# Optimization experiments

Measured on AMD Instinct MI355X. Metric: run time of the kernel, lower is better.

## Reference

```python
import jax, jax.numpy as jnp
import numpy as np

# Config matching init_kwargs: input_shape=(512,512,28), stride=2
M, N, L = 512, 512, 28
STRIDE = 2
B = 8


def setup_inputs() -> dict:
    key = jax.random.key(0)
    kx, kp = jax.random.split(key)
    x = jax.random.normal(kx, (B, L, M, N), dtype=jnp.float32)
    # phi = (1 + sign(randn)) / 2  -> binary {0,1} mask of shape (M, N)
    phi = (jax.random.normal(kp, (M, N)) > 0).astype(jnp.float32)
    return {"x": x, "phi": phi}


def reference(x, phi):
    """CASSI forward: get_transpose(get_measurement(x, phi), phi, mask_mul=True).

    x:   (b, L, M, N) hyperspectral cube
    phi: (M, N) coded aperture, broadcast across L bands
    """
    b, l, m, n = x.shape
    n_out = n + STRIDE * (l - 1)

    # --- get_measurement: mask-multiply then per-band shift-and-accumulate ---
    y1 = x * phi[None, None, :, :]                      # (b, L, M, N)
    # column index each (band, col) lands in after dispersion shift
    scat_idx = (STRIDE * jnp.arange(l)[:, None] + jnp.arange(n)[None, :]).reshape(-1)  # (L*N,)
    y1f = y1.transpose(0, 2, 1, 3).reshape(b, m, l * n)  # (b, M, L*N)
    y2 = jnp.zeros((b, m, n_out), dtype=x.dtype).at[:, :, scat_idx].add(y1f)  # (b, M, Nout)
    # y_norm=False: no normalization

    # --- get_transpose: gather shifted windows (width = y.shape[-2] = M) ---
    gat_idx = STRIDE * jnp.arange(l)[:, None] + jnp.arange(m)[None, :]  # (L, M)
    xt = y2[:, :, gat_idx]             # (b, M, L, M)
    xt = jnp.moveaxis(xt, 2, 1)        # (b, L, M, M)
    return xt * phi[None, None, :, :]  # mask_mul=True
```

## Files before the change

### kernel.cpp

```cpp
#include <hip/hip_runtime.h>


#define M_DIM 512
#define N_DIM 512
#define L_DIM 28
#define B_DIM 8
#define MN_DIM (M_DIM * N_DIM)
#define NT 14
#define U_DIM 14

typedef float v2f __attribute__((ext_vector_type(2)));
typedef float v4f __attribute__((ext_vector_type(4)));

__global__ __launch_bounds__(128) void cassi_fwd_kernel(
    const float* __restrict__ x, const float* __restrict__ phi,
    float* __restrict__ out)
{
    __shared__ __align__(16) float sphi[N_DIM];
    __shared__ __align__(16) float sy2[576];

    const int t  = threadIdx.x;
    const int bm = blockIdx.x;
    const int b  = bm >> 9;
    const int m  = bm & 511;

    const float* xrow = x + (size_t)b * L_DIM * MN_DIM + (size_t)m * N_DIM;

    v4f pq = *(const v4f*)(phi + (size_t)m * N_DIM + 4 * t);
    *(v4f*)&sphi[4 * t] = pq;
    __syncthreads();

    const bool lane0 = ((t & 63) == 0);

    v4f acc  = {0.f, 0.f, 0.f, 0.f};
    v4f acct = {0.f, 0.f, 0.f, 0.f};

#pragma unroll
    for (int u = 0; u < U_DIM; ++u) {
        const int s  = t - u;
        const int sc = s < 0 ? 0 : s;
        const float* re = xrow + (size_t)(2 * u) * MN_DIM;
        const float* ro = xrow + (size_t)(2 * u + 1) * MN_DIM;
        v4f xe = *(const v4f*)(re + 4 * sc);
        v4f xo = *(const v4f*)(ro + 4 * sc);
        v4f P  = *(const v4f*)(&sphi[4 * sc]);
        v4f ze = xe * P;
        v4f zo = xo * P;

        if (s >= 0) acc += ze;

        float lo0 = __shfl_up(zo.z, 1, 64);
        float lo1 = __shfl_up(zo.w, 1, 64);
        if (lane0 && s >= 1) {
            v2f xl = *(const v2f*)(ro + 4 * s - 2);
            v2f pl = *(const v2f*)(&sphi[4 * s - 2]);
            lo0 = xl.x * pl.x;
            lo1 = xl.y * pl.y;
        }
        if (s >= 1) { acc.x += lo0;  acc.y += lo1; }
        if (s >= 0) { acc.z += zo.x; acc.w += zo.y; }

        if (t < NT) {
            if (u == t) {
                v2f xl = *(const v2f*)(ro + 510);
                v2f pl = *(const v2f*)(&sphi[510]);
                acct.x += xl.x * pl.x;
                acct.y += xl.y * pl.y;
            } else if (u > t) {
                const int n0 = 512 + 4 * t - 4 * u;
                v4f xte = *(const v4f*)(re + n0);
                v4f Pt  = *(const v4f*)(&sphi[n0]);
                acct += xte * Pt;
                v2f xa = *(const v2f*)(ro + n0 - 2);
                v2f pa = *(const v2f*)(&sphi[n0 - 2]);
                v2f xb = *(const v2f*)(ro + n0);
                acct.x += xa.x * pa.x;
                acct.y += xa.y * pa.y;
                acct.z += xb.x * Pt.x;
                acct.w += xb.y * Pt.y;
            }
        }
    }

    *(v4f*)&sy2[4 * t] = acc;
    if (t < NT) *(v4f*)&sy2[512 + 4 * t] = acct;
    __syncthreads();

    float* orow = out + (size_t)b * L_DIM * MN_DIM + (size_t)m * N_DIM;
    const float* sy = &sy2[0];
#pragma unroll
    for (int l = 0; l < L_DIM; ++l) {
        v2f ya = *(const v2f*)(sy + 2 * l + 4 * t);
        v2f yb = *(const v2f*)(sy + 2 * l + 4 * t + 2);
        v4f o;
        o.x = pq.x * ya.x;
        o.y = pq.y * ya.y;
        o.z = pq.z * yb.x;
        o.w = pq.w * yb.y;
        __builtin_nontemporal_store(o, (v4f*)(orow + (size_t)l * MN_DIM + 4 * t));
    }
}

extern "C" void kernel_launch(void* const* d_in, const int* in_sizes, int n_in,
                              void* d_out, int out_size, void* d_ws, size_t ws_size,
                              hipStream_t stream) {
    const float* x   = (const float*)d_in[0];
    const float* phi = (const float*)d_in[1];
    float* out       = (float*)d_out;
    cassi_fwd_kernel<<<dim3(B_DIM * M_DIM), dim3(128), 0, stream>>>(x, phi, out);
}
```

Baseline: 393.8 us.

## Split fused kernel into y2 reduction pass and separate expand pass via workspace

Splits the fused kernel into two. The first kernel computes the dispersed measurement rows y2 and writes them to a workspace buffer. The second kernel reads y2 and phi and writes each output band, with blocks ordered by band so that consecutive stores are contiguous. The goal is more streaming-friendly write patterns and more parallelism in the expand phase, at the cost of an extra kernel launch and a round trip of y2 through global memory. If the workspace is missing or too small, the original fused kernel runs instead.

```diff
diff --git a/kernel.cpp b/kernel.cpp
--- a/kernel.cpp
+++ b/kernel.cpp
@@ -8,16 +8,17 @@
 #define MN_DIM (M_DIM * N_DIM)
 #define NT 14
 #define U_DIM 14
+#define YSTRIDE 576
+#define MB 8
 
 typedef float v2f __attribute__((ext_vector_type(2)));
 typedef float v4f __attribute__((ext_vector_type(4)));
 
-__global__ __launch_bounds__(128) void cassi_fwd_kernel(
+__global__ __launch_bounds__(128) void cassi_y2_kernel(
     const float* __restrict__ x, const float* __restrict__ phi,
-    float* __restrict__ out)
+    float* __restrict__ y2w)
 {
     __shared__ __align__(16) float sphi[N_DIM];
-    __shared__ __align__(16) float sy2[576];
 
     const int t  = threadIdx.x;
     const int bm = blockIdx.x;
@@ -82,6 +83,114 @@
         }
     }
 
+    float* yrow = y2w + (size_t)bm * YSTRIDE;
+    *(v4f*)(yrow + 4 * t) = acc;
+    if (t < NT) *(v4f*)(yrow + 512 + 4 * t) = acct;
+}
+
+__global__ __launch_bounds__(256) void cassi_expand_kernel(
+    const float* __restrict__ y2w, const float* __restrict__ phi,
+    float* __restrict__ out)
+{
+    const int bid = blockIdx.x;
+    const int mc  = bid & 63;
+    const int bl  = bid >> 6;
+    const int l   = bl % L_DIM;
+    const int b   = bl / L_DIM;
+    const int m0  = mc * MB;
+
+    const int c = threadIdx.x & 31;
+    const int r = threadIdx.x >> 5;
+    const int m = m0 + r;
+
+    const float* yrow = y2w + (size_t)((b << 9) | m) * YSTRIDE + 2 * l;
+    const float* prow = phi + (size_t)m * N_DIM;
+    float* orow = out + ((size_t)b * L_DIM + l) * MN_DIM + (size_t)m * N_DIM;
+
+#pragma unroll
+    for (int q = 0; q < 4; ++q) {
+        const int n0 = 4 * c + 128 * q;
+        v4f P  = *(const v4f*)(prow + n0);
+        v2f ya = *(const v2f*)(yrow + n0);
+        v2f yb = *(const v2f*)(yrow + n0 + 2);
+        v4f o;
+        o.x = P.x * ya.x;
+        o.y = P.y * ya.y;
+        o.z = P.z * yb.x;
+        o.w = P.w * yb.y;
+        __builtin_nontemporal_store(o, (v4f*)(orow + n0));
+    }
+}
+
+__global__ __launch_bounds__(128) void cassi_fwd_kernel(
+    const float* __restrict__ x, const float* __restrict__ phi,
+    float* __restrict__ out)
+{
+    __shared__ __align__(16) float sphi[N_DIM];
+    __shared__ __align__(16) float sy2[576];
+
+    const int t  = threadIdx.x;
+    const int bm = blockIdx.x;
+    const int b  = bm >> 9;
+    const int m  = bm & 511;
+
+    const float* xrow = x + (size_t)b * L_DIM * MN_DIM + (size_t)m * N_DIM;
+
+    v4f pq = *(const v4f*)(phi + (size_t)m * N_DIM + 4 * t);
+    *(v4f*)&sphi[4 * t] = pq;
+    __syncthreads();
+
+    const bool lane0 = ((t & 63) == 0);
+    v4f acc  = {0.f, 0.f, 0.f, 0.f};
+    v4f acct = {0.f, 0.f, 0.f, 0.f};
+
+#pragma unroll
+    for (int u = 0; u < U_DIM; ++u) {
+        const int s  = t - u;
+        const int sc = s < 0 ? 0 : s;
+        const float* re = xrow + (size_t)(2 * u) * MN_DIM;
+        const float* ro = xrow + (size_t)(2 * u + 1) * MN_DIM;
+        v4f xe = *(const v4f*)(re + 4 * sc);
+        v4f xo = *(const v4f*)(ro + 4 * sc);
+        v4f P  = *(const v4f*)(&sphi[4 * sc]);
+        v4f ze = xe * P;
+        v4f zo = xo * P;
+
+        if (s >= 0) acc += ze;
+
+        float lo0 = __shfl_up(zo.z, 1, 64);
+        float lo1 = __shfl_up(zo.w, 1, 64);
+        if (lane0 && s >= 1) {
+            v2f xl = *(const v2f*)(ro + 4 * s - 2);
+            v2f pl = *(const v2f*)(&sphi[4 * s - 2]);
+            lo0 = xl.x * pl.x;
+            lo1 = xl.y * pl.y;
+        }
+        if (s >= 1) { acc.x += lo0;  acc.y += lo1; }
+        if (s >= 0) { acc.z += zo.x; acc.w += zo.y; }
+
+        if (t < NT) {
+            if (u == t) {
+                v2f xl = *(const v2f*)(ro + 510);
+                v2f pl = *(const v2f*)(&sphi[510]);
+                acct.x += xl.x * pl.x;
+                acct.y += xl.y * pl.y;
+            } else if (u > t) {
+                const int n0 = 512 + 4 * t - 4 * u;
+                v4f xte = *(const v4f*)(re + n0);
+                v4f Pt  = *(const v4f*)(&sphi[n0]);
+                acct += xte * Pt;
+                v2f xa = *(const v2f*)(ro + n0 - 2);
+                v2f pa = *(const v2f*)(&sphi[n0 - 2]);
+                v2f xb = *(const v2f*)(ro + n0);
+                acct.x += xa.x * pa.x;
+                acct.y += xa.y * pa.y;
+                acct.z += xb.x * Pt.x;
+                acct.w += xb.y * Pt.y;
+            }
+        }
+    }
+
     *(v4f*)&sy2[4 * t] = acc;
     if (t < NT) *(v4f*)&sy2[512 + 4 * t] = acct;
     __syncthreads();
@@ -107,5 +216,13 @@
     const float* x   = (const float*)d_in[0];
     const float* phi = (const float*)d_in[1];
     float* out       = (float*)d_out;
-    cassi_fwd_kernel<<<dim3(B_DIM * M_DIM), dim3(128), 0, stream>>>(x, phi, out);
-}
+
+    const size_t ws_needed = (size_t)B_DIM * M_DIM * YSTRIDE * sizeof(float);
+    if (d_ws != nullptr && ws_size >= ws_needed) {
+        float* y2w = (float*)d_ws;
+        cassi_y2_kernel<<<dim3(B_DIM * M_DIM), dim3(128), 0, stream>>>(x, phi, y2w);
+        cassi_expand_kernel<<<dim3(B_DIM * L_DIM * (M_DIM / MB)), dim3(256), 0, stream>>>(y2w, phi, out);
+    } else {
+        cassi_fwd_kernel<<<dim3(B_DIM * M_DIM), dim3(128), 0, stream>>>(x, phi, out);
+    }
+}
```

Measured after the change: 387.3 us. About the same (-1.6%).
